# Performance work log

Hardware: AMD Instinct MI355X
Metric: run time of the kernel (lower is better)

Reference implementation:

```python
import jax, jax.numpy as jnp
from jax import lax
import numpy as np

KPAD = 2  # padding for 5x5 kernel, 'same' output

def setup_inputs() -> dict:
    key = jax.random.key(0)
    x = jax.random.normal(key, (16, 8, 512, 512), dtype=jnp.float32)
    # fixed 5x5 averaging kernel, matching torch.ones(5,5)/25
    weight = jnp.ones((1, 1, 5, 5), dtype=jnp.float32) / 25.0
    return {"x": x, "weight": weight}

def reference(x, weight):
    # Per-channel (depthwise) 5x5 box blur. The torch code loops conv2d over
    # split channels; a single grouped conv with feature_group_count=C is the
    # same math in one fused op.
    C = x.shape[1]
    k = jnp.tile(weight, (C, 1, 1, 1))  # (C,1,5,5) OIHW with groups=C
    return lax.conv_general_dilated(
        x, k,
        window_strides=(1, 1),
        padding=[(KPAD, KPAD), (KPAD, KPAD)],
        dimension_numbers=("NCHW", "OIHW", "NCHW"),
        feature_group_count=C,
    )
```

## Files before the change

### kernel.cpp

```cpp
#include <hip/hip_runtime.h>


#define H 512
#define W 512
#define TH 16
#define LROWS (TH + 4)
#define LSTRIDE (W + 8)

__global__ __launch_bounds__(256) void avefilter_kernel(
    const float* __restrict__ x, const float* __restrict__ wgt,
    float* __restrict__ out) {
    __shared__ float smem[LROWS * LSTRIDE];

    const int tid   = threadIdx.x;
    const int r0    = blockIdx.x * TH;
    const int plane = blockIdx.y;

    const float* in   = x   + (size_t)plane * (H * W);
    float*       outp = out + (size_t)plane * (H * W);
    const float scale = wgt[0];

    for (int i = tid; i < LROWS * 8; i += 256) {
        int lr = i >> 3;
        int c  = i & 7;
        int lc = (c < 4) ? c : (W + c);
        smem[lr * LSTRIDE + lc] = 0.0f;
    }

    for (int i = tid; i < LROWS * (W / 4); i += 256) {
        int lr = i >> 7;
        int vc = i & 127;
        int gr = r0 - 2 + lr;
        float4 v = make_float4(0.f, 0.f, 0.f, 0.f);
        if (gr >= 0 && gr < H) {
            v = ((const float4*)(in + (size_t)gr * W))[vc];
        }
        ((float4*)(smem + lr * LSTRIDE + 4))[vc] = v;
    }
    __syncthreads();

    #pragma unroll
    for (int ci = 0; ci < 2; ++ci) {
        const int xcol = tid + ci * 256;
        const float* bcol = smem + xcol + 2;

        float h[5];
        #pragma unroll
        for (int i = 0; i < 5; ++i) {
            const float* b = bcol + i * LSTRIDE;
            h[i] = b[0] + b[1] + b[2] + b[3] + b[4];
        }

        #pragma unroll
        for (int r = 0; r < TH; ++r) {
            float s = h[0] + h[1] + h[2] + h[3] + h[4];
            outp[(size_t)(r0 + r) * W + xcol] = s * scale;
            if (r < TH - 1) {
                const float* b = bcol + (r + 5) * LSTRIDE;
                h[r % 5] = b[0] + b[1] + b[2] + b[3] + b[4];
            }
        }
    }
}

extern "C" void kernel_launch(void* const* d_in, const int* in_sizes, int n_in,
                              void* d_out, int out_size, void* d_ws, size_t ws_size,
                              hipStream_t stream) {
    const float* x   = (const float*)d_in[0];
    const float* wgt = (const float*)d_in[1];
    float* out = (float*)d_out;

    dim3 grid(H / TH, 16 * 8);
    dim3 block(256);
    avefilter_kernel<<<grid, block, 0, stream>>>(x, wgt, out);
}
```

Measured before the change: 239.7 us.

## Replace shared-memory tile with register running vertical sums over row bands

Drops the LDS staging and __syncthreads. Each thread now owns two adjacent columns and keeps running vertical column sums in registers. Every output row adds the incoming row and subtracts the outgoing row, reading both straight from global memory with float2 loads plus neighbour halos, over 32-row bands. This removes the shared-memory traffic and the 4-row halo re-load per 16-row tile. In exchange it reads each input row twice (add and subtract), relies on L1/L2 for the overlapping neighbour loads, and adds floating-point rounding drift from the add/subtract running sums.

```diff
diff --git a/kernel.cpp b/kernel.cpp
--- a/kernel.cpp
+++ b/kernel.cpp
@@ -3,63 +3,76 @@
 
 #define H 512
 #define W 512
-#define TH 16
-#define LROWS (TH + 4)
-#define LSTRIDE (W + 8)
+#define RB 32
+#define NB (H / RB)
 
-__global__ __launch_bounds__(256) void avefilter_kernel(
+__device__ __forceinline__ float2 ld2(const float* p) {
+    return *reinterpret_cast<const float2*>(p);
+}
+
+__global__ __launch_bounds__(256, 8) void avefilter_kernel(
     const float* __restrict__ x, const float* __restrict__ wgt,
-    float* __restrict__ out) {
-    __shared__ float smem[LROWS * LSTRIDE];
+    float* __restrict__ out)
+{
+    const int t     = threadIdx.x;
+    const int band  = blockIdx.x;
+    const int plane = blockIdx.y;
+    const int c0    = t * 2;
+    const int r0    = band * RB;
 
-    const int tid   = threadIdx.x;
-    const int r0    = blockIdx.x * TH;
-    const int plane = blockIdx.y;
-
-    const float* in   = x   + (size_t)plane * (H * W);
-    float*       outp = out + (size_t)plane * (H * W);
+    const float* in = x + (size_t)plane * (H * W);
     const float scale = wgt[0];
 
-    for (int i = tid; i < LROWS * 8; i += 256) {
-        int lr = i >> 3;
-        int c  = i & 7;
-        int lc = (c < 4) ? c : (W + c);
-        smem[lr * LSTRIDE + lc] = 0.0f;
+    const bool hL = (t != 0);
+    const bool hR = (t != 255);
+    const float2 z = make_float2(0.f, 0.f);
+
+    float2 sl = z, sm = z, sr = z;
+
+    for (int rr = r0 - 2; rr <= r0 + 1; ++rr) {
+        if (rr >= 0) {
+            const float* p = in + (size_t)rr * W + c0;
+            float2 a = hL ? ld2(p - 2) : z;
+            float2 b = ld2(p);
+            float2 c = hR ? ld2(p + 2) : z;
+            sl.x += a.x; sl.y += a.y;
+            sm.x += b.x; sm.y += b.y;
+            sr.x += c.x; sr.y += c.y;
+        }
     }
 
-    for (int i = tid; i < LROWS * (W / 4); i += 256) {
-        int lr = i >> 7;
-        int vc = i & 127;
-        int gr = r0 - 2 + lr;
-        float4 v = make_float4(0.f, 0.f, 0.f, 0.f);
-        if (gr >= 0 && gr < H) {
-            v = ((const float4*)(in + (size_t)gr * W))[vc];
-        }
-        ((float4*)(smem + lr * LSTRIDE + 4))[vc] = v;
-    }
-    __syncthreads();
+    const float* pn = in + (size_t)(r0 + 2) * W + c0;
+    const float* po = in + (size_t)(r0 - 2) * W + c0;
+    float* op = out + (size_t)plane * (H * W) + (size_t)r0 * W + c0;
 
-    #pragma unroll
-    for (int ci = 0; ci < 2; ++ci) {
-        const int xcol = tid + ci * 256;
-        const float* bcol = smem + xcol + 2;
+    #pragma unroll 4
+    for (int i = 0; i < RB; ++i) {
+        const int r = r0 + i;
 
-        float h[5];
-        #pragma unroll
-        for (int i = 0; i < 5; ++i) {
-            const float* b = bcol + i * LSTRIDE;
-            h[i] = b[0] + b[1] + b[2] + b[3] + b[4];
+        if (r + 2 < H) {
+            float2 a = hL ? ld2(pn - 2) : z;
+            float2 b = ld2(pn);
+            float2 c = hR ? ld2(pn + 2) : z;
+            sl.x += a.x; sl.y += a.y;
+            sm.x += b.x; sm.y += b.y;
+            sr.x += c.x; sr.y += c.y;
         }
 
-        #pragma unroll
-        for (int r = 0; r < TH; ++r) {
-            float s = h[0] + h[1] + h[2] + h[3] + h[4];
-            outp[(size_t)(r0 + r) * W + xcol] = s * scale;
-            if (r < TH - 1) {
-                const float* b = bcol + (r + 5) * LSTRIDE;
-                h[r % 5] = b[0] + b[1] + b[2] + b[3] + b[4];
-            }
+        float a1 = sl.y + sm.x + sm.y;
+        float h0 = (sl.x + a1) + sr.x;
+        float h1 = (a1 + sr.x) + sr.y;
+        *reinterpret_cast<float2*>(op) = make_float2(h0 * scale, h1 * scale);
+
+        if (r - 2 >= 0) {
+            float2 a = hL ? ld2(po - 2) : z;
+            float2 b = ld2(po);
+            float2 c = hR ? ld2(po + 2) : z;
+            sl.x -= a.x; sl.y -= a.y;
+            sm.x -= b.x; sm.y -= b.y;
+            sr.x -= c.x; sr.y -= c.y;
         }
+
+        pn += W; po += W; op += W;
     }
 }
 
@@ -70,7 +83,7 @@
     const float* wgt = (const float*)d_in[1];
     float* out = (float*)d_out;
 
-    dim3 grid(H / TH, 16 * 8);
+    dim3 grid(NB, 16 * 8);
     dim3 block(256);
     avefilter_kernel<<<grid, block, 0, stream>>>(x, wgt, out);
 }
```

After: 290.0 us. 21.0% more time.
